# Kernel tuning notes

Hardware: AMD Instinct MI355X
Metric: run time of the kernel (lower is better)

Reference implementation:

```python
import jax, jax.numpy as jnp
import numpy as np

B, TE, TD, E, H, V, A, MAXOOV = 8, 400, 100, 128, 256, 50000, 612, 50
VEXT = V + MAXOOV


def setup_inputs():
    key = jax.random.key(0)
    it = iter(jax.random.split(key, 40))
    def nrm(shape, s=0.05):
        return jax.random.normal(next(it), shape, jnp.float32) * s
    inp = {
        "encoder_tokens": jax.random.randint(next(it), (B, TE), 0, V, dtype=jnp.int32),
        "decoder_tokens": jax.random.randint(next(it), (B, TD), 0, V, dtype=jnp.int32),
        "encoder_ext_tokens": jax.random.randint(next(it), (B, TE), 0, VEXT, dtype=jnp.int32),
        "encoder_mask": jnp.ones((B, TE), jnp.float32),
        "embedding": nrm((V, E)),
        "Wih_f": nrm((E, 4 * H)), "Whh_f": nrm((H, 4 * H)), "b_f": jnp.zeros((4 * H,), jnp.float32),
        "Wih_b": nrm((E, 4 * H)), "Whh_b": nrm((H, 4 * H)), "b_b": jnp.zeros((4 * H,), jnp.float32),
        "Wred": nrm((2 * H, H)), "bred": jnp.zeros((H,), jnp.float32),
        "Wenc_feat": nrm((2 * H, A)), "benc_feat": jnp.zeros((A,), jnp.float32),
        "v": nrm((A,), 1.0),
        "Wx": nrm((E + 2 * H, E)), "bx": jnp.zeros((E,), jnp.float32),
        "Wih_d": nrm((E, 4 * H)), "Whh_d": nrm((H, 4 * H)), "b_d": jnp.zeros((4 * H,), jnp.float32),
        "Wdf": nrm((TD, 2 * H, A)), "bdf": jnp.zeros((TD, A), jnp.float32),
        "Wpg": nrm((2 * H + H + H + E, 1)), "bpg": jnp.zeros((1,), jnp.float32),
        "Wout": nrm((H + 2 * H, H)), "bout": jnp.zeros((H,), jnp.float32),
        "Wv": nrm((H, V)), "bv": jnp.zeros((V,), jnp.float32),
    }
    return inp


def _lstm(xs, Wih, Whh, b):
    # xs: [T, B, E] -> outputs [T, B, H], final (h, c)
    def step(carry, x):
        h, c = carry
        g = x @ Wih + h @ Whh + b
        i, f, gg, o = jnp.split(g, 4, axis=-1)  # torch gate order i,f,g,o
        c = jax.nn.sigmoid(f) * c + jax.nn.sigmoid(i) * jnp.tanh(gg)
        h = jax.nn.sigmoid(o) * jnp.tanh(c)
        return (h, c), h
    z = jnp.zeros((xs.shape[1], Whh.shape[0]), xs.dtype)
    (hT, cT), hs = jax.lax.scan(step, (z, z), xs)
    return hs, hT, cT


def reference(encoder_tokens, decoder_tokens, encoder_ext_tokens, encoder_mask,
              embedding, Wih_f, Whh_f, b_f, Wih_b, Whh_b, b_b, Wred, bred,
              Wenc_feat, benc_feat, v, Wx, bx, Wih_d, Whh_d, b_d, Wdf, bdf,
              Wpg, bpg, Wout, bout, Wv, bv):
    # ---- bidirectional LSTM encoder (full-length sequences, mask == 1) ----
    enc_emb = embedding[encoder_tokens]               # [B, TE, E]
    xs = enc_emb.transpose(1, 0, 2)                   # [TE, B, E]
    hf, hTf, cTf = _lstm(xs, Wih_f, Whh_f, b_f)
    hb_rev, hTb, cTb = _lstm(xs[::-1], Wih_b, Whh_b, b_b)
    hb = hb_rev[::-1]
    enc_out = jnp.concatenate([hf, hb], -1).transpose(1, 0, 2)  # [B, TE, 2H]

    # ---- state reducer (original uses reduce_h_layer for BOTH h and c) ----
    h0 = jax.nn.relu(jnp.concatenate([hTf, hTb], -1) @ Wred + bred)
    c0 = jax.nn.relu(jnp.concatenate([cTf, cTb], -1) @ Wred + bred)

    # ---- 1x1 conv == linear on encoder states ----
    enc_feat = enc_out @ Wenc_feat + benc_feat        # [B, TE, A]

    dec_emb = embedding[decoder_tokens].transpose(1, 0, 2)  # [TD, B, E]

    def dec_step(carry, xs_t):
        h, c, ctx = carry
        emb_t, Wdf_t, bdf_t = xs_t
        x = jnp.concatenate([emb_t, ctx], -1) @ Wx + bx          # [B, E]
        g = x @ Wih_d + h @ Whh_d + b_d
        i, f, gg, o = jnp.split(g, 4, axis=-1)
        c = jax.nn.sigmoid(f) * c + jax.nn.sigmoid(i) * jnp.tanh(gg)
        h = jax.nn.sigmoid(o) * jnp.tanh(c)
        dec_feat = jnp.concatenate([h, c], -1) @ Wdf_t + bdf_t   # [B, A] (per-step weights)
        e = jnp.einsum('a,bta->bt', v, jnp.tanh(enc_feat + dec_feat[:, None, :]))
        attn = jax.nn.softmax(e, axis=-1) * encoder_mask
        attn = attn / attn.sum(-1, keepdims=True)
        ctx = jnp.einsum('bt,btd->bd', attn, enc_out)            # [B, 2H]
        p_gen = jax.nn.sigmoid(jnp.concatenate([ctx, h, c, x], -1) @ Wpg + bpg)  # [B, 1]
        out = jnp.concatenate([h, ctx], -1) @ Wout + bout        # [B, H]
        return (h, c, ctx), (out, attn, p_gen)

    ctx0 = jnp.zeros((enc_out.shape[0], 2 * H), enc_out.dtype)
    _, (outs, attns, pgens) = jax.lax.scan(dec_step, (h0, c0, ctx0), (dec_emb, Wdf, bdf))
    # outs [TD,B,H], attns [TD,B,TE], pgens [TD,B,1]

    # ---- pointer-generator mixture over extended vocab ----
    vocab_dist = jax.nn.softmax(outs @ Wv + bv, axis=-1)         # [TD, B, V]
    vocab_dist = pgens * vocab_dist
    attn_w = (1.0 - pgens) * attns                               # [TD, B, TE]

    def scatter_one(a, idx):
        return jnp.zeros((VEXT,), a.dtype).at[idx].add(a)
    copy_dist = jax.vmap(jax.vmap(scatter_one, in_axes=(0, 0)), in_axes=(0, None))(
        attn_w, encoder_ext_tokens)                              # [TD, B, VEXT]

    extra = jnp.zeros(vocab_dist.shape[:2] + (MAXOOV,), vocab_dist.dtype)
    final = jnp.concatenate([vocab_dist, extra], -1) + copy_dist # [TD, B, VEXT]
    return final
```

## Files before the change

### kernel.cpp

```cpp
#include <hip/hip_runtime.h>

#define DEVI __device__ __forceinline__

constexpr int B_ = 8, TE_ = 400, TD_ = 100, E_ = 128, H_ = 256;
constexpr int A_ = 612, V_ = 50000, VEXT_ = 50050;
constexpr int H4_ = 1024, H2_ = 512;
constexpr int NS_ = 16, SLW_ = 40;

constexpr size_t OFS_HBF  = 0;
constexpr size_t OFS_HBB  = 4096;
constexpr size_t OFS_CT   = 8192;
constexpr size_t OFS_CHC  = 12288;
constexpr size_t OFS_PG   = 32896;
constexpr size_t OFS_SROW = 33696;
constexpr size_t OFS_FLG  = 34496;
constexpr size_t OFS_ATT  = 35520;
constexpr size_t OFS_EO   = 355520;
constexpr size_t OFS_OUTS = OFS_EO;
constexpr size_t OFS_EF   = OFS_EO + (size_t)B_*TE_*H2_;

constexpr size_t DO_GINF = 0;
constexpr size_t DO_GINB = DO_GINF + (size_t)TE_*B_*H4_;
constexpr size_t DO_GDEC = DO_GINB + (size_t)TE_*B_*H4_;
constexpr size_t DO_XPRE = DO_GDEC + (size_t)TD_*B_*H4_;
constexpr size_t DO_CTXH = DO_XPRE + (size_t)TD_*B_*E_;
constexpr size_t DO_HCH  = DO_CTXH + (size_t)TD_*B_*H2_;
constexpr size_t DO_WCG  = DO_HCH + (size_t)TD_*B_*H2_;
constexpr size_t DO_EOWT = DO_WCG + (size_t)H2_*H4_;
constexpr size_t DO_EPB  = DO_EOWT + (size_t)B_*H4_*TE_;

#if defined(__has_builtin)
#if __has_builtin(__builtin_amdgcn_rcpf)
#define HAS_RCPF 1
#endif
#endif

DEVI float rcp_fast(float x) {
#ifdef HAS_RCPF
  return __builtin_amdgcn_rcpf(x);
#else
  return 1.0f / x;
#endif
}

DEVI float sigm(float x) { return rcp_fast(1.0f + __expf(-x)); }
DEVI float tanh_fast(float x) {
  float e = __expf(2.0f * x);
  return 1.0f - 2.0f * rcp_fast(e + 1.0f);
}

DEVI float ld_at(const float* p) {
  unsigned u = __hip_atomic_load((const unsigned*)p, __ATOMIC_RELAXED, __HIP_MEMORY_SCOPE_AGENT);
  return __uint_as_float(u);
}
DEVI void st_at(float* p, float v) {
  __hip_atomic_store((unsigned*)p, __float_as_uint(v), __ATOMIC_RELAXED, __HIP_MEMORY_SCOPE_AGENT);
}

#define WAIT_VM() do { asm volatile("s_waitcnt vmcnt(0)" ::: "memory"); \
                       __builtin_amdgcn_sched_barrier(0); } while (0)

DEVI float wave_max(float v) {
#pragma unroll
  for (int o = 32; o; o >>= 1) v = fmaxf(v, __shfl_xor(v, o));
  return v;
}
DEVI float wave_sum(float v) {
#pragma unroll
  for (int o = 32; o; o >>= 1) v += __shfl_xor(v, o);
  return v;
}

DEVI void flag_bar(unsigned* flags, int ncheck, int slot, unsigned ep, int stride) {
  __syncthreads();
  if (threadIdx.x == 0) {
    asm volatile("s_waitcnt vmcnt(0)" ::: "memory");
    __hip_atomic_store(&flags[slot * stride], ep, __ATOMIC_RELAXED, __HIP_MEMORY_SCOPE_AGENT);
  }
  if ((int)threadIdx.x < ncheck) {
    while (__hip_atomic_load(&flags[threadIdx.x * stride], __ATOMIC_RELAXED,
                             __HIP_MEMORY_SCOPE_AGENT) < ep) {
      __builtin_amdgcn_s_sleep(2);
    }
  }
  __syncthreads();
  asm volatile("" ::: "memory");
}

__global__ __launch_bounds__(256) void k0_wcg(
    const float* __restrict__ Wx, const float* __restrict__ Wih_d, float* __restrict__ dob)
{
  __shared__ float AsT[32 * 64];
  __shared__ float Bsh[32 * 64];
  const float* Am = Wx + 128 * 128;
  float* C = dob + DO_WCG;
  const int ct = blockIdx.x, rt = blockIdx.y, tid = threadIdx.x;
  const int c0 = ct * 64, r0 = rt * 64;
  const int tx = tid & 15, ty = tid >> 4;
  float4 acc0 = make_float4(0,0,0,0), acc1 = acc0, acc2 = acc0, acc3 = acc0;
  for (int kc = 0; kc < 4; ++kc) {
#pragma unroll
    for (int i = 0; i < 2; ++i) {
      int q = tid * 2 + i;
      int r = q >> 3, kq = q & 7;
      float4 v = *(const float4*)&Am[(size_t)(r0 + r) * 128 + kc * 32 + kq * 4];
      AsT[(kq * 4 + 0) * 64 + r] = v.x; AsT[(kq * 4 + 1) * 64 + r] = v.y;
      AsT[(kq * 4 + 2) * 64 + r] = v.z; AsT[(kq * 4 + 3) * 64 + r] = v.w;
    }
#pragma unroll
    for (int i = 0; i < 2; ++i) {
      int q = tid * 2 + i;
      int kk = q >> 4, cq = q & 15;
      *(float4*)&Bsh[kk * 64 + cq * 4] =
          *(const float4*)&Wih_d[(size_t)(kc * 32 + kk) * H4_ + c0 + cq * 4];
    }
    __syncthreads();
#pragma unroll
    for (int kk = 0; kk < 32; ++kk) {
      float4 w4 = *(float4*)&Bsh[kk * 64 + tx * 4];
      const float* ar = &AsT[kk * 64 + ty * 4];
      acc0.x += ar[0]*w4.x; acc0.y += ar[0]*w4.y; acc0.z += ar[0]*w4.z; acc0.w += ar[0]*w4.w;
      acc1.x += ar[1]*w4.x; acc1.y += ar[1]*w4.y; acc1.z += ar[1]*w4.z; acc1.w += ar[1]*w4.w;
      acc2.x += ar[2]*w4.x; acc2.y += ar[2]*w4.y; acc2.z += ar[2]*w4.z; acc2.w += ar[2]*w4.w;
      acc3.x += ar[3]*w4.x; acc3.y += ar[3]*w4.y; acc3.z += ar[3]*w4.z; acc3.w += ar[3]*w4.w;
    }
    __syncthreads();
  }
  float4 r4[4] = {acc0, acc1, acc2, acc3};
#pragma unroll
  for (int i = 0; i < 4; ++i)
    *(float4*)&C[(size_t)(r0 + ty * 4 + i) * H4_ + c0 + tx * 4] = r4[i];
}

__global__ __launch_bounds__(256) void k1_embed_gates(
    const int* __restrict__ etok, const float* __restrict__ emb,
    const float* __restrict__ Wih_f, const float* __restrict__ b_f,
    const float* __restrict__ Wih_b, const float* __restrict__ b_b,
    float* __restrict__ gin_f, float* __restrict__ gin_b, float* __restrict__ ws)
{
  __shared__ float er[8 * 128];
  const int t = blockIdx.x, tid = threadIdx.x;
  if (t == 0) {
    for (int i = tid; i < 8192; i += 256) ws[OFS_HBF + i] = 0.0f;
    unsigned* f = (unsigned*)(ws + OFS_FLG);
    for (int i = tid; i < 1024; i += 256) f[i] = 0u;
  }
  for (int i = tid; i < 1024; i += 256) {
    int b = i >> 7, e = i & 127;
    er[i] = emb[(size_t)etok[b * TE_ + t] * E_ + e];
  }
  __syncthreads();
  float bfv[4], bbv[4];
#pragma unroll
  for (int g = 0; g < 4; ++g) { bfv[g] = b_f[g * H_ + tid]; bbv[g] = b_b[g * H_ + tid]; }
  float af[32], ab[32];
#pragma unroll
  for (int i = 0; i < 32; ++i) { af[i] = bfv[i & 3]; ab[i] = bbv[i & 3]; }
  for (int e = 0; e < E_; ++e) {
    float wf[4], wb[4];
#pragma unroll
    for (int g = 0; g < 4; ++g) {
      wf[g] = Wih_f[(size_t)e * H4_ + g * H_ + tid];
      wb[g] = Wih_b[(size_t)e * H4_ + g * H_ + tid];
    }
#pragma unroll
    for (int b = 0; b < 8; ++b) {
      float x = er[b * 128 + e];
#pragma unroll
      for (int g = 0; g < 4; ++g) { af[b * 4 + g] += x * wf[g]; ab[b * 4 + g] += x * wb[g]; }
    }
  }
#pragma unroll
  for (int b = 0; b < 8; ++b)
#pragma unroll
    for (int g = 0; g < 4; ++g) {
      gin_f[((size_t)t * 8 + b) * H4_ + g * H_ + tid] = af[b * 4 + g];
      gin_b[((size_t)t * 8 + b) * H4_ + g * H_ + tid] = ab[b * 4 + g];
    }
}

__global__ __launch_bounds__(256) void k1d_dec_pre(
    const int* __restrict__ dtok, const float* __restrict__ emb,
    const float* __restrict__ Wx, const float* __restrict__ bx,
    const float* __restrict__ Wih_d, const float* __restrict__ b_d,
    float* __restrict__ dob)
{
  __shared__ float er[8 * 128];
  __shared__ float xl[8 * 128];
  const int t = blockIdx.x, tid = threadIdx.x;
  for (int i = tid; i < 1024; i += 256) {
    int b = i >> 7, e = i & 127;
    er[i] = emb[(size_t)dtok[b * TD_ + t] * E_ + e];
  }
  __syncthreads();
  {
    const int col = tid & 127, bh = tid >> 7;
#pragma unroll
    for (int ii = 0; ii < 4; ++ii) {
      int b = bh + (ii << 1);
      float acc = bx[col];
      for (int k = 0; k < 128; ++k) acc += er[b * 128 + k] * Wx[(size_t)k * E_ + col];
      xl[b * 128 + col] = acc;
      dob[DO_XPRE + ((size_t)t * 8 + b) * E_ + col] = acc;
    }
  }
  __syncthreads();
  float bv[4];
#pragma unroll
  for (int g = 0; g < 4; ++g) bv[g] = b_d[g * H_ + tid];
  float af[32];
#pragma unroll
  for (int i = 0; i < 32; ++i) af[i] = bv[i & 3];
  for (int e = 0; e < E_; ++e) {
    float w[4];
#pragma unroll
    for (int g = 0; g < 4; ++g) w[g] = Wih_d[(size_t)e * H4_ + g * H_ + tid];
#pragma unroll
    for (int b = 0; b < 8; ++b) {
      float x = xl[b * 128 + e];
#pragma unroll
      for (int g = 0; g < 4; ++g) af[b * 4 + g] += x * w[g];
    }
  }
#pragma unroll
  for (int b = 0; b < 8; ++b)
#pragma unroll
    for (int g = 0; g < 4; ++g)
      dob[DO_GDEC + ((size_t)t * 8 + b) * H4_ + g * H_ + tid] = af[b * 4 + g];
}

__global__ __launch_bounds__(256, 1) void k2_encoder_scan(
    const float* __restrict__ gin_f, const float* __restrict__ gin_b,
    const float* __restrict__ Whh_f, const float* __restrict__ Whh_b,
    float* __restrict__ ws)
{
  __shared__ float sm[4096];
  const int bid = blockIdx.x, tid = threadIdx.x;
  const int dir = bid >> 5, c0 = (bid & 31) * 8;
  const float* Whh = dir ? Whh_b : Whh_f;
  const float* gin = dir ? gin_b : gin_f;
  float* hb = ws + (dir ? OFS_HBB : OFS_HBF);
  float* cT = ws + OFS_CT;
  float* eo = ws + OFS_EO;
  unsigned* flg = (unsigned*)(ws + OFS_FLG) + (dir ? 128 : 0);
  const int slot = bid & 31;

  const int jl = tid >> 3, kg = tid & 7;
  const int gt = jl >> 3, hcl = jl & 7;
  const int jcol = gt * H_ + c0 + hcl;
  float wreg[32];
#pragma unroll
  for (int kk = 0; kk < 32; ++kk) wreg[kk] = Whh[(size_t)(kg + kk * 8) * H4_ + jcol];

  const int uhc = tid >> 3, ub = tid & 7;
  float c_reg = 0.0f;
  unsigned ep = 0;

  for (int t = 0; t < TE_; ++t) {
    const int te = dir ? (TE_ - 1 - t) : t;
    float* hrd = hb + (t & 1) * 2048;
    float* hwr = hb + ((t & 1) ^ 1) * 2048;
    float gpre[4] = {0, 0, 0, 0};
    if (tid < 64) {
#pragma unroll
      for (int gg = 0; gg < 4; ++gg)
        gpre[gg] = gin[((size_t)te * 8 + ub) * H4_ + gg * H_ + c0 + uhc];
    }
    {
      float4 v0, v1;
      const float* a0 = &hrd[tid * 8];
      const float* a1 = &hrd[tid * 8 + 4];
      asm volatile(
          "global_load_dwordx4 %0, %2, off sc0 sc1\n\t"
          "global_load_dwordx4 %1, %3, off sc0 sc1"
          : "=&v"(v0), "=&v"(v1) : "v"(a0), "v"(a1));
      WAIT_VM();
      *(float4*)&sm[tid * 8] = v0;
      *(float4*)&sm[tid * 8 + 4] = v1;
    }
    __syncthreads();
    float acc[8] = {0, 0, 0, 0, 0, 0, 0, 0};
#pragma unroll
    for (int kk = 0; kk < 32; ++kk) {
      float w = wreg[kk];
      const float* hp = &sm[(kg + kk * 8) * 8];
#pragma unroll
      for (int b = 0; b < 8; ++b) acc[b] += hp[b] * w;
    }
    float* part = sm + 2048;
    *(float4*)&part[(jl * 8 + kg) * 8]     = make_float4(acc[0], acc[1], acc[2], acc[3]);
    *(float4*)&part[(jl * 8 + kg) * 8 + 4] = make_float4(acc[4], acc[5], acc[6], acc[7]);
    __syncthreads();
    if (tid < 64) {
      float g[4];
#pragma unroll
      for (int gg = 0; gg < 4; ++gg) {
        float s = gpre[gg];
#pragma unroll
        for (int k2 = 0; k2 < 8; ++k2) s += part[((gg * 8 + uhc) * 8 + k2) * 8 + ub];
        g[gg] = s;
      }
      float ci = sigm(g[0]), cf = sigm(g[1]), cg = tanh_fast(g[2]), co = sigm(g[3]);
      c_reg = cf * c_reg + ci * cg;
      float hn = co * tanh_fast(c_reg);
      st_at(&hwr[(c0 + uhc) * 8 + ub], hn);
      eo[((size_t)ub * TE_ + te) * H2_ + dir * H_ + c0 + uhc] = hn;
      if (t == TE_ - 1) cT[ub * H2_ + dir * H_ + c0 + uhc] = c_reg;
    }
    ep++; flag_bar(flg, 32, slot, ep, 4);
  }
}

__global__ __launch_bounds__(256) void k3_encfeat(
    const float* __restrict__ eo, const float* __restrict__ Wef,
    const float* __restrict__ bef, float* __restrict__ ef)
{
  __shared__ float AsT[32 * 64];
  __shared__ float Wsh[32 * 64];
  const int ct = blockIdx.x, rt = blockIdx.y, tid = threadIdx.x;
  const int c0 = ct * 64, r0 = rt * 64;
  const int tx = tid & 15, ty = tid >> 4;
  float4 acc0 = make_float4(0,0,0,0), acc1 = acc0, acc2 = acc0, acc3 = acc0;
  for (int kc = 0; kc < 16; ++kc) {
#pragma unroll
    for (int i = 0; i < 2; ++i) {
      int q = tid * 2 + i;
      int r = q >> 3, kq = q & 7;
      float4 v = *(const float4*)&eo[(size_t)(r0 + r) * H2_ + kc * 32 + kq * 4];
      AsT[(kq * 4 + 0) * 64 + r] = v.x; AsT[(kq * 4 + 1) * 64 + r] = v.y;
      AsT[(kq * 4 + 2) * 64 + r] = v.z; AsT[(kq * 4 + 3) * 64 + r] = v.w;
    }
#pragma unroll
    for (int i = 0; i < 2; ++i) {
      int q = tid * 2 + i;
      int kk = q >> 4, cq = q & 15;
      int col = c0 + cq * 4;
      float4 v = make_float4(0,0,0,0);
      if (col < A_) v = *(const float4*)&Wef[(size_t)(kc * 32 + kk) * A_ + col];
      *(float4*)&Wsh[kk * 64 + cq * 4] = v;
    }
    __syncthreads();
#pragma unroll
    for (int kk = 0; kk < 32; ++kk) {
      float4 w4 = *(float4*)&Wsh[kk * 64 + tx * 4];
      const float* ar = &AsT[kk * 64 + ty * 4];
      acc0.x += ar[0]*w4.x; acc0.y += ar[0]*w4.y; acc0.z += ar[0]*w4.z; acc0.w += ar[0]*w4.w;
      acc1.x += ar[1]*w4.x; acc1.y += ar[1]*w4.y; acc1.z += ar[1]*w4.z; acc1.w += ar[1]*w4.w;
      acc2.x += ar[2]*w4.x; acc2.y += ar[2]*w4.y; acc2.z += ar[2]*w4.z; acc2.w += ar[2]*w4.w;
      acc3.x += ar[3]*w4.x; acc3.y += ar[3]*w4.y; acc3.z += ar[3]*w4.z; acc3.w += ar[3]*w4.w;
    }
    __syncthreads();
  }
  const int col = c0 + tx * 4;
  if (col < A_) {
    float4 bb = *(const float4*)&bef[col];
    float4 r4[4] = {acc0, acc1, acc2, acc3};
#pragma unroll
    for (int i = 0; i < 4; ++i) {
      int row = r0 + ty * 4 + i;
      float4 o = make_float4(r4[i].x + bb.x, r4[i].y + bb.y, r4[i].z + bb.z, r4[i].w + bb.w);
      *(float4*)&ef[(size_t)row * A_ + col] = o;
    }
  }
}

__global__ __launch_bounds__(256) void k3b_eowt(
    const float* __restrict__ eo, const float* __restrict__ dob_c, float* __restrict__ dob)
{
  __shared__ float Wt[32 * 64];
  __shared__ float Et[32 * 40];
  const float* Wcg = dob_c + DO_WCG;
  float* eoWT = dob + DO_EOWT;
  const int jt = blockIdx.x, tt = blockIdx.y, b = blockIdx.z, tid = threadIdx.x;
  const int j0 = jt * 64, te0 = tt * 40;
  const int j_l = tid & 63, tq = tid >> 6;
  float acc[10];
#pragma unroll
  for (int u = 0; u < 10; ++u) acc[u] = 0.0f;
  for (int kc = 0; kc < 16; ++kc) {
#pragma unroll
    for (int i = 0; i < 2; ++i) {
      int q = tid * 2 + i;
      int kk = q >> 4, j4 = q & 15;
      *(float4*)&Wt[kk * 64 + j4 * 4] =
          *(const float4*)&Wcg[(size_t)(kc * 32 + kk) * H4_ + j0 + j4 * 4];
    }
#pragma unroll
    for (int i = 0; i < 2; ++i) {
      int q = tid + i * 256;
      if (q < 320) {
        int te_l = q >> 3, kq = q & 7;
        float4 v = *(const float4*)&eo[((size_t)b * TE_ + te0 + te_l) * H2_ + kc * 32 + kq * 4];
        Et[(kq * 4 + 0) * 40 + te_l] = v.x; Et[(kq * 4 + 1) * 40 + te_l] = v.y;
        Et[(kq * 4 + 2) * 40 + te_l] = v.z; Et[(kq * 4 + 3) * 40 + te_l] = v.w;
      }
    }
    __syncthreads();
#pragma unroll
    for (int kk = 0; kk < 32; ++kk) {
      float w = Wt[kk * 64 + j_l];
      const float* ep2 = &Et[kk * 40 + tq * 10];
#pragma unroll
      for (int u = 0; u < 10; ++u) acc[u] += w * ep2[u];
    }
    __syncthreads();
  }
  float* outp = &eoWT[((size_t)b * H4_ + j0 + j_l) * TE_ + te0 + tq * 10];
#pragma unroll
  for (int u = 0; u < 10; ++u) outp[u] = acc[u];
}

__global__ __launch_bounds__(512, 1) void k4_decoder(
    const float* __restrict__ maskp,
    const float* __restrict__ Wred, const float* __restrict__ bred,
    const float* __restrict__ Whh_d,
    const float* __restrict__ Wdf, const float* __restrict__ bdf,
    const float* __restrict__ vvec, float* __restrict__ ws, float* __restrict__ dob)
{
  __shared__ float eoW[TE_ * 64];
  __shared__ float eu[TE_];
  __shared__ float hcL[512];
  __shared__ float red[16];
  __shared__ float gdL[64];
  __shared__ float gl[64];
  __shared__ float pgl[64 * 9];
  __shared__ float prt[1280];
  __shared__ float dfl[48];
  __shared__ float bdfL[48];
  __shared__ float vvL[48];

  float* chc = ws + OFS_CHC;
  float* att = ws + OFS_ATT;
  const float* efG = ws + OFS_EF;
  const float* hbf = ws + OFS_HBF;
  const float* hbb = ws + OFS_HBB;
  const float* cT  = ws + OFS_CT;
  unsigned* flgF = (unsigned*)(ws + OFS_FLG) + 256;
  const float* gdec = dob + DO_GDEC;
  const float* eoWT = dob + DO_EOWT;
  float* epb = dob + DO_EPB;
  float* hch = dob + DO_HCH;
  const int bid = blockIdx.x, tid = threadIdx.x;
  const int b = bid >> 4, s = bid & 15;
  unsigned* flgG = (unsigned*)(ws + OFS_FLG) + 512 + b * 64;
  const int a0 = s * SLW_, w = (s == 15) ? 12 : SLW_;
  const int nq = w >> 2;

  for (int i = tid; i < 64 * 100; i += 512) {
    int jgi = i / 100, c = i - jgi * 100;
    int jreal = (jgi >> 4) * 256 + s * 16 + (jgi & 15);
    float4 v = *(const float4*)&eoWT[((size_t)b * H4_ + jreal) * TE_ + c * 4];
    eoW[(c * 4 + 0) * 64 + jgi] = v.x;
    eoW[(c * 4 + 1) * 64 + jgi] = v.y;
    eoW[(c * 4 + 2) * 64 + jgi] = v.z;
    eoW[(c * 4 + 3) * 64 + jgi] = v.w;
  }
  const int jg = tid & 63, l8 = tid >> 6;
  const int jreal = (jg >> 4) * 256 + s * 16 + (jg & 15);
  float wreg[32];
#pragma unroll
  for (int kk = 0; kk < 32; ++kk)
    wreg[kk] = Whh_d[(size_t)(l8 + kk * 8) * H4_ + jreal];
  if (tid < w) vvL[tid] = vvec[a0 + tid];

  if (bid < 32) {
    const int isC = bid >> 4, pb = (bid >> 1) & 7, half = bid & 1;
    if (tid < 512)
      hcL[tid] = isC ? cT[pb * H2_ + tid]
                     : (tid < H_ ? hbf[tid * 8 + pb] : hbb[(tid - H_) * 8 + pb]);
    __syncthreads();
    {
      const int col_l = tid & 127, ks = tid >> 7;
      float acc = 0.0f;
      for (int kk = 0; kk < 128; ++kk) {
        int k = ks * 128 + kk;
        acc += hcL[k] * Wred[(size_t)k * H_ + half * 128 + col_l];
      }
      prt[ks * 128 + col_l] = acc;
    }
    __syncthreads();
    if (tid < 128) {
      float v2 = fmaxf(prt[tid] + prt[128 + tid] + prt[256 + tid] + prt[384 + tid] +
                       bred[half * 128 + tid], 0.0f);
      st_at(&chc[pb * H2_ + isC * H_ + half * 128 + tid], v2);
    }
  } else {
    float dm = 0.0f;
#pragma unroll
    for (int i = 0; i < 7; ++i) {
      int f = (bid - 32) * 3264 + i * 512 + tid;
      if (i * 512 + tid < 3264 && f < H2_ * A_) dm += Wdf[f];
    }
    asm volatile("" :: "v"(dm));
  }
  unsigned ep = 1;
  flag_bar(flgF, 128, bid, ep, 2);

  float c_reg = 0.0f;
  if (tid < 16) c_reg = ld_at(&chc[b * H2_ + H_ + s * 16 + tid]);
  unsigned epg = 0;

  for (int t = 0; t <= TD_; ++t) {
    const int cur = t & 1, nxt = cur ^ 1;

    {
      const int teA = (tid < TE_) ? tid : TE_ - 1;
      const int tcl = (t < TD_) ? t : TD_ - 1;
      const float* ae = &epb[((size_t)b * TE_ + teA) * 16];
      const float* ah = &chc[cur * 4096 + b * H2_ + (tid & 63) * 4];
      const int gi = tid & 15;
      const float* agd = &gdec[((size_t)tcl * 8 + b) * H4_ +
                               (gi >> 2) * 256 + s * 16 + (gi & 3) * 4];
      float4 v0, v1, v2, v3, vh, vgd;
      asm volatile(
          "global_load_dwordx4 %0, %6, off sc0 sc1\n\t"
          "global_load_dwordx4 %1, %7, off sc0 sc1\n\t"
          "global_load_dwordx4 %2, %8, off sc0 sc1\n\t"
          "global_load_dwordx4 %3, %9, off sc0 sc1\n\t"
          "global_load_dwordx4 %4, %10, off sc0 sc1\n\t"
          "global_load_dwordx4 %5, %11, off sc0 sc1"
          : "=&v"(v0), "=&v"(v1), "=&v"(v2), "=&v"(v3), "=&v"(vh), "=&v"(vgd)
          : "v"(ae), "v"(ae + 4), "v"(ae + 8), "v"(ae + 12), "v"(ah), "v"(agd));
      WAIT_VM();
      if (t > 0 && tid < TE_)
        eu[tid] = (v0.x + v0.y + v0.z + v0.w) + (v1.x + v1.y + v1.z + v1.w) +
                  (v2.x + v2.y + v2.z + v2.w) + (v3.x + v3.y + v3.z + v3.w);
      if (tid < 64) *(float4*)&hcL[tid * 4] = vh;
      if (tid < 16) *(float4*)&gdL[(gi >> 2) * 16 + (gi & 3) * 4] = vgd;
      __syncthreads();

      float inv = 0.0f;
      if (t > 0) {
        float m = (tid < TE_) ? eu[tid] : -3.4e38f;
        m = wave_max(m);
        if ((tid & 63) == 0) red[tid >> 6] = m;
        __syncthreads();
        m = red[0];
#pragma unroll
        for (int i = 1; i < 8; ++i) m = fmaxf(m, red[i]);
        float u = 0.0f;
        if (tid < TE_) {
          u = __expf(eu[tid] - m) * maskp[b * TE_ + tid];
          eu[tid] = u;
        }
        float sl = wave_sum(u);
        if ((tid & 63) == 0) red[8 + (tid >> 6)] = sl;
        __syncthreads();
        float S = 0.0f;
#pragma unroll
        for (int i = 0; i < 8; ++i) S += red[8 + i];
        inv = rcp_fast(S);
      }

      if (t > 0 && s == 0 && tid < TE_)
        att[((size_t)(t - 1) * 8 + b) * TE_ + tid] = eu[tid] * inv;

      if (t < TD_) {
        float accG = 0.0f, accW = 0.0f;
        if (t > 0) {
          for (int te = l8; te < TE_; te += 8)
            accG += eoW[te * 64 + jg] * eu[te];
        }
#pragma unroll
        for (int kk = 0; kk < 32; ++kk)
          accW += wreg[kk] * hcL[l8 + kk * 8];
        pgl[jg * 9 + l8] = accG * inv + accW;
        __syncthreads();
        if (tid < 64) {
          float sg = gdL[tid];
#pragma unroll
          for (int l = 0; l < 8; ++l) sg += pgl[tid * 9 + l];
          gl[tid] = sg;
        }
        __syncthreads();
        if (tid < 16) {
          float g0 = gl[tid], g1 = gl[16 + tid], g2 = gl[32 + tid], g3 = gl[48 + tid];
          float ci = sigm(g0), cf = sigm(g1), cg = tanh_fast(g2), co = sigm(g3);
          c_reg = cf * c_reg + ci * cg;
          float hn = co * tanh_fast(c_reg);
          int hc = s * 16 + tid;
          st_at(&chc[nxt * 4096 + b * H2_ + hc], hn);
          st_at(&chc[nxt * 4096 + b * H2_ + H_ + hc], c_reg);
          hch[((size_t)t * 8 + b) * H2_ + hc] = hn;
          hch[((size_t)t * 8 + b) * H2_ + H_ + hc] = c_reg;
        }
      }
    }
    if (t == TD_) break;
    epg++; flag_bar(flgG, 16, s, epg, 4);

    {
      {
        const float* ahc = &chc[nxt * 4096 + b * H2_ + (tid & 127) * 4];
        const int cl = (tid < 10) ? tid : 9;
        const float* abf = &bdf[(size_t)t * A_ + a0 + cl * 4];
        float4 vhc, vbf;
        asm volatile(
            "global_load_dwordx4 %0, %2, off sc0 sc1\n\t"
            "global_load_dwordx4 %1, %3, off sc0 sc1"
            : "=&v"(vhc), "=&v"(vbf) : "v"(ahc), "v"(abf));
        WAIT_VM();
        if (tid < 128) *(float4*)&hcL[tid * 4] = vhc;
        if (tid < 10) *(float4*)&bdfL[tid * 4] = vbf;
      }
      __syncthreads();

      const float* wp = Wdf + (size_t)t * H2_ * A_;
      {
        const int kq = tid >> 4, al = tid & 15;
        if (al < nq) {
          float4 a4 = make_float4(0, 0, 0, 0);
          const float* wpc = wp + a0 + al * 4;
#pragma unroll
          for (int i = 0; i < 16; ++i) {
            int k = kq * 16 + i;
            float4 w4 = *(const float4*)&wpc[(size_t)k * A_];
            float hv = hcL[k];
            a4.x += hv * w4.x; a4.y += hv * w4.y; a4.z += hv * w4.z; a4.w += hv * w4.w;
          }
          *(float4*)&prt[(kq * 10 + al) * 4] = a4;
        }
      }
      float dm = 0.0f;
      if (t + 1 < TD_) {
        const float* wp1 = Wdf + (size_t)(t + 1) * H2_ * A_ + (size_t)tid * A_ + a0;
#pragma unroll
        for (int q = 0; q < 10; ++q) {
          float4 vx = *(const float4*)&wp1[q * 4];
          dm += vx.x + vx.y + vx.z + vx.w;
        }
      }
      __syncthreads();
      if (tid < w) {
        float ssum = bdfL[tid];
        const int c4 = tid >> 2, r = tid & 3;
#pragma unroll
        for (int kq = 0; kq < 32; ++kq) ssum += prt[(kq * 10 + c4) * 4 + r];
        dfl[tid] = ssum;
      }
      __syncthreads();

      if (tid < TE_) {
        const float* efp = &efG[((size_t)b * TE_ + tid) * A_ + a0];
        float acc = 0.0f;
        for (int q = 0; q < nq; ++q) {
          float4 e4 = *(const float4*)&efp[q * 4];
          const float* dd = &dfl[q * 4];
          const float* vv = &vvL[q * 4];
          acc += vv[0] * tanh_fast(e4.x + dd[0]);
          acc += vv[1] * tanh_fast(e4.y + dd[1]);
          acc += vv[2] * tanh_fast(e4.z + dd[2]);
          acc += vv[3] * tanh_fast(e4.w + dd[3]);
        }
        st_at(&epb[((size_t)b * TE_ + tid) * 16 + s], acc);
      }
      asm volatile("" :: "v"(dm));
    }
    epg++; flag_bar(flgG, 16, s, epg, 4);
  }
}

__global__ __launch_bounds__(256) void k4c_ctx(
    const float* __restrict__ ws, float* __restrict__ dob)
{
  __shared__ float AsT[32 * 64];
  __shared__ float Bsh[32 * 64];
  const float* att = ws + OFS_ATT;
  const float* eo  = ws + OFS_EO;
  float* ctxh = dob + DO_CTXH;
  const int ct = blockIdx.x, rt = blockIdx.y, b = blockIdx.z, tid = threadIdx.x;
  const int c0 = ct * 64, r0 = rt * 64;
  const int tx = tid & 15, ty = tid >> 4;
  float4 acc0 = make_float4(0,0,0,0), acc1 = acc0, acc2 = acc0, acc3 = acc0;
  for (int kc = 0; kc < 13; ++kc) {
#pragma unroll
    for (int i = 0; i < 2; ++i) {
      int q = tid * 2 + i;
      int r = q >> 3, kq = q & 7;
      int k = kc * 32 + kq * 4;
      float4 v = make_float4(0, 0, 0, 0);
      if (k < TE_ && r0 + r < TD_)
        v = *(const float4*)&att[((size_t)(r0 + r) * 8 + b) * TE_ + k];
      AsT[(kq * 4 + 0) * 64 + r] = v.x; AsT[(kq * 4 + 1) * 64 + r] = v.y;
      AsT[(kq * 4 + 2) * 64 + r] = v.z; AsT[(kq * 4 + 3) * 64 + r] = v.w;
    }
#pragma unroll
    for (int i = 0; i < 2; ++i) {
      int q = tid * 2 + i;
      int kk = q >> 4, cq = q & 15;
      int k = kc * 32 + kk;
      float4 v = make_float4(0, 0, 0, 0);
      if (k < TE_) v = *(const float4*)&eo[((size_t)b * TE_ + k) * H2_ + c0 + cq * 4];
      *(float4*)&Bsh[kk * 64 + cq * 4] = v;
    }
    __syncthreads();
#pragma unroll
    for (int kk = 0; kk < 32; ++kk) {
      float4 w4 = *(float4*)&Bsh[kk * 64 + tx * 4];
      const float* ar = &AsT[kk * 64 + ty * 4];
      acc0.x += ar[0]*w4.x; acc0.y += ar[0]*w4.y; acc0.z += ar[0]*w4.z; acc0.w += ar[0]*w4.w;
      acc1.x += ar[1]*w4.x; acc1.y += ar[1]*w4.y; acc1.z += ar[1]*w4.z; acc1.w += ar[1]*w4.w;
      acc2.x += ar[2]*w4.x; acc2.y += ar[2]*w4.y; acc2.z += ar[2]*w4.z; acc2.w += ar[2]*w4.w;
      acc3.x += ar[3]*w4.x; acc3.y += ar[3]*w4.y; acc3.z += ar[3]*w4.z; acc3.w += ar[3]*w4.w;
    }
    __syncthreads();
  }
  float4 r4[4] = {acc0, acc1, acc2, acc3};
#pragma unroll
  for (int i = 0; i < 4; ++i) {
    int row = r0 + ty * 4 + i;
    if (row < TD_)
      *(float4*)&ctxh[((size_t)row * 8 + b) * H2_ + c0 + tx * 4] = r4[i];
  }
}

__global__ __launch_bounds__(256) void k4b_post(
    const float* __restrict__ Wx, const float* __restrict__ Wout, const float* __restrict__ bout,
    const float* __restrict__ Wpg, const float* __restrict__ bpg,
    float* __restrict__ ws, const float* __restrict__ dob)
{
  __shared__ float hcl[4096], ctxl[4096], cpl[4096], xl[1024], red2[256];
  const int t = blockIdx.x, tid = threadIdx.x;
  const float* hch  = dob + DO_HCH;
  const float* ctxh = dob + DO_CTXH;
  const float* xpre = dob + DO_XPRE;
  for (int i = tid; i < 4096; i += 256) {
    hcl[i]  = hch[(size_t)t * 4096 + i];
    ctxl[i] = ctxh[(size_t)t * 4096 + i];
    cpl[i]  = t ? ctxh[(size_t)(t - 1) * 4096 + i] : 0.0f;
  }
  __syncthreads();
  {
    const int col = tid & 127, bh = tid >> 7;
#pragma unroll
    for (int ii = 0; ii < 4; ++ii) {
      int b = bh + (ii << 1);
      float acc = xpre[(size_t)t * 1024 + b * E_ + col];
      for (int k = 0; k < H2_; ++k) acc += cpl[b * H2_ + k] * Wx[(size_t)(128 + k) * E_ + col];
      xl[b * E_ + col] = acc;
    }
  }
  __syncthreads();
  {
    const int col = tid;
    for (int b = 0; b < 8; ++b) {
      float acc = bout[col];
      for (int k = 0; k < 768; ++k)
        acc += (k < H_ ? hcl[b * H2_ + k] : ctxl[b * H2_ + (k - H_)]) * Wout[(size_t)k * H_ + col];
      ws[OFS_OUTS + ((size_t)t * 8 + b) * H_ + col] = acc;
    }
  }
  {
    const int b = tid >> 5, sg = tid & 31;
    float acc = 0.0f;
    for (int j = 0; j < 36; ++j) {
      int k = sg * 36 + j;
      float xv;
      if (k < H2_)       xv = ctxl[b * H2_ + k];
      else if (k < 768)  xv = hcl[b * H2_ + (k - H2_)];
      else if (k < 1024) xv = hcl[b * H2_ + H_ + (k - 768)];
      else               xv = xl[b * E_ + (k - 1024)];
      acc += xv * Wpg[k];
    }
    red2[tid] = acc;
    __syncthreads();
    if (tid < 8) {
      float s = 0.0f;
      for (int k2 = 0; k2 < 32; ++k2) s += red2[tid * 32 + k2];
      ws[OFS_PG + t * 8 + tid] = sigm(s + bpg[0]);
    }
  }
}

__global__ __launch_bounds__(256) void k5a_logits(
    const float* __restrict__ outs, const float* __restrict__ Wv,
    const float* __restrict__ bv, float* __restrict__ out)
{
  __shared__ float aT[32 * 64];
  __shared__ float wl[32 * 256];
  const int ct = blockIdx.x, rt = blockIdx.y, tid = threadIdx.x;
  const int r0 = rt * 64, c0 = ct * 256;
  const int cq = tid & 63, rg = tid >> 6;
  float4 acc[16];
#pragma unroll
  for (int i = 0; i < 16; ++i) acc[i] = make_float4(0, 0, 0, 0);
  for (int kc = 0; kc < 8; ++kc) {
#pragma unroll
    for (int i = 0; i < 2; ++i) {
      int q = tid * 2 + i;
      int r = q >> 3, kq = q & 7;
      float4 v = make_float4(0, 0, 0, 0);
      if (r0 + r < 800) v = *(const float4*)&outs[(size_t)(r0 + r) * H_ + kc * 32 + kq * 4];
      aT[(kq * 4 + 0) * 64 + r] = v.x; aT[(kq * 4 + 1) * 64 + r] = v.y;
      aT[(kq * 4 + 2) * 64 + r] = v.z; aT[(kq * 4 + 3) * 64 + r] = v.w;
    }
#pragma unroll
    for (int i = 0; i < 8; ++i) {
      int q = tid + i * 256;
      int kk = q >> 6, c4 = q & 63;
      int col = c0 + c4 * 4;
      float4 v = make_float4(0, 0, 0, 0);
      if (col < V_) v = *(const float4*)&Wv[(size_t)(kc * 32 + kk) * V_ + col];
      *(float4*)&wl[kk * 256 + c4 * 4] = v;
    }
    __syncthreads();
#pragma unroll
    for (int kk = 0; kk < 32; ++kk) {
      float4 w4 = *(float4*)&wl[kk * 256 + cq * 4];
      const float* ar = &aT[kk * 64 + rg * 16];
#pragma unroll
      for (int rr = 0; rr < 16; ++rr) {
        float a = ar[rr];
        acc[rr].x += a * w4.x; acc[rr].y += a * w4.y;
        acc[rr].z += a * w4.z; acc[rr].w += a * w4.w;
      }
    }
    __syncthreads();
  }
  const int col = c0 + cq * 4;
  if (col < V_) {
    float4 bb = *(const float4*)&bv[col];
#pragma unroll
    for (int rr = 0; rr < 16; ++rr) {
      int row = r0 + rg * 16 + rr;
      if (row < 800) {
        float2 lo = make_float2(acc[rr].x + bb.x, acc[rr].y + bb.y);
        float2 hi = make_float2(acc[rr].z + bb.z, acc[rr].w + bb.w);
        *(float2*)&out[(size_t)row * VEXT_ + col] = lo;
        *(float2*)&out[(size_t)row * VEXT_ + col + 2] = hi;
      }
    }
  }
}

__global__ __launch_bounds__(256) void k5b_rowsum(const float* __restrict__ out, float* __restrict__ Srow)
{
  __shared__ float red[256];
  const int r = blockIdx.x, tid = threadIdx.x;
  const float* base = out + (size_t)r * VEXT_;
  float s = 0.0f;
  for (int i = tid; i < V_ / 2; i += 256) {
    float2 v = *(const float2*)&base[i * 2];
    s += __expf(v.x) + __expf(v.y);
  }
  red[tid] = s; __syncthreads();
  for (int st = 128; st > 0; st >>= 1) { if (tid < st) red[tid] += red[tid + st]; __syncthreads(); }
  if (tid == 0) Srow[r] = red[0];
}

__global__ __launch_bounds__(256) void k5c_final(
    float* __restrict__ out, const float* __restrict__ Srow, const float* __restrict__ pg)
{
  const int cc = blockIdx.x, r = blockIdx.y, tid = threadIdx.x;
  const float scale = pg[r] * rcp_fast(Srow[r]);
  float* base = out + (size_t)r * VEXT_;
#pragma unroll
  for (int i = 0; i < 4; ++i) {
    int col = cc * 2048 + i * 512 + tid * 2;
    if (col < V_) {
      float2 v = *(float2*)&base[col];
      v.x = __expf(v.x) * scale; v.y = __expf(v.y) * scale;
      *(float2*)&base[col] = v;
    } else if (col < VEXT_) {
      *(float2*)&base[col] = make_float2(0.0f, 0.0f);
    }
  }
}

__global__ __launch_bounds__(256) void k5d_scatter(
    float* __restrict__ out, const float* __restrict__ ws, const int* __restrict__ ext)
{
  const int r = blockIdx.x, tid = threadIdx.x;
  const int b = r & 7;
  const float* at = ws + OFS_ATT + (size_t)r * TE_;
  const float w = 1.0f - ws[OFS_PG + r];
  float* base = out + (size_t)r * VEXT_;
  for (int i = tid; i < TE_; i += 256)
    atomicAdd(&base[ext[b * TE_ + i]], w * at[i]);
}

extern "C" void kernel_launch(void* const* d_in, const int* in_sizes, int n_in,
                              void* d_out, int out_size, void* d_ws, size_t ws_size,
                              hipStream_t stream) {
  const int*   etok  = (const int*)d_in[0];
  const int*   dtok  = (const int*)d_in[1];
  const int*   ext   = (const int*)d_in[2];
  const float* maskp = (const float*)d_in[3];
  const float* emb   = (const float*)d_in[4];
  const float* Wih_f = (const float*)d_in[5];
  const float* Whh_f = (const float*)d_in[6];
  const float* b_f   = (const float*)d_in[7];
  const float* Wih_b = (const float*)d_in[8];
  const float* Whh_b = (const float*)d_in[9];
  const float* b_b   = (const float*)d_in[10];
  const float* Wred  = (const float*)d_in[11];
  const float* bred  = (const float*)d_in[12];
  const float* Wef   = (const float*)d_in[13];
  const float* bef   = (const float*)d_in[14];
  const float* vvec  = (const float*)d_in[15];
  const float* Wx    = (const float*)d_in[16];
  const float* bx    = (const float*)d_in[17];
  const float* Wih_d = (const float*)d_in[18];
  const float* Whh_d = (const float*)d_in[19];
  const float* b_d   = (const float*)d_in[20];
  const float* Wdf   = (const float*)d_in[21];
  const float* bdf   = (const float*)d_in[22];
  const float* Wpg   = (const float*)d_in[23];
  const float* bpg   = (const float*)d_in[24];
  const float* Wout  = (const float*)d_in[25];
  const float* bout  = (const float*)d_in[26];
  const float* Wv    = (const float*)d_in[27];
  const float* bv    = (const float*)d_in[28];
  float* out = (float*)d_out;
  float* wsf = (float*)d_ws;
  float* dob = out;

  float* gin_f = dob + DO_GINF;
  float* gin_b = dob + DO_GINB;

  k1_embed_gates<<<400, 256, 0, stream>>>(etok, emb, Wih_f, b_f, Wih_b, b_b, gin_f, gin_b, wsf);
  k0_wcg<<<dim3(16, 8), 256, 0, stream>>>(Wx, Wih_d, dob);
  k1d_dec_pre<<<100, 256, 0, stream>>>(dtok, emb, Wx, bx, Wih_d, b_d, dob);

  {
    void* args2[5] = {(void*)&gin_f, (void*)&gin_b, (void*)&Whh_f, (void*)&Whh_b, (void*)&wsf};
    if (hipLaunchCooperativeKernel((void*)k2_encoder_scan, dim3(64), dim3(256), args2, 0, stream) != hipSuccess)
      k2_encoder_scan<<<64, 256, 0, stream>>>(gin_f, gin_b, Whh_f, Whh_b, wsf);
  }

  k3_encfeat<<<dim3(10, 50), 256, 0, stream>>>(wsf + OFS_EO, Wef, bef, wsf + OFS_EF);
  k3b_eowt<<<dim3(16, 10, 8), 256, 0, stream>>>(wsf + OFS_EO, dob, dob);

  {
    void* args4[9] = {(void*)&maskp, (void*)&Wred, (void*)&bred, (void*)&Whh_d,
                      (void*)&Wdf, (void*)&bdf, (void*)&vvec, (void*)&wsf, (void*)&dob};
    if (hipLaunchCooperativeKernel((void*)k4_decoder, dim3(128), dim3(512), args4, 0, stream) != hipSuccess)
      k4_decoder<<<128, 512, 0, stream>>>(maskp, Wred, bred, Whh_d, Wdf, bdf, vvec, wsf, dob);
  }

  k4c_ctx<<<dim3(8, 2, 8), 256, 0, stream>>>(wsf, dob);
  k4b_post<<<100, 256, 0, stream>>>(Wx, Wout, bout, Wpg, bpg, wsf, dob);

  k5a_logits<<<dim3(196, 13), 256, 0, stream>>>(wsf + OFS_OUTS, Wv, bv, out);
  k5b_rowsum<<<800, 256, 0, stream>>>(out, wsf + OFS_SROW);
  k5c_final<<<dim3(25, 800), 256, 0, stream>>>(out, wsf + OFS_SROW, wsf + OFS_PG);
  k5d_scatter<<<800, 256, 0, stream>>>(out, wsf, ext);
}
```

Before: 3.766 ms.

## Fuse encoder input projection into scan, redistribute decoder loads, swap logits grid order

The separate embedding/input-gate kernel is removed. Its work moves into the cooperative encoder scan, which keeps Wih columns in registers and gathers embeddings per step. This drops the large gate-preactivation buffer write and read, but adds per-step input-projection work on the serial critical path. The decoder also spreads the attention store and the Wdf prefetch-touch across more threads, and the logits grid swaps its axes so row tiles vary fastest.

```diff
diff --git a/kernel.cpp b/kernel.cpp
--- a/kernel.cpp
+++ b/kernel.cpp
@@ -19,9 +19,7 @@
 constexpr size_t OFS_OUTS = OFS_EO;
 constexpr size_t OFS_EF   = OFS_EO + (size_t)B_*TE_*H2_;
 
-constexpr size_t DO_GINF = 0;
-constexpr size_t DO_GINB = DO_GINF + (size_t)TE_*B_*H4_;
-constexpr size_t DO_GDEC = DO_GINB + (size_t)TE_*B_*H4_;
+constexpr size_t DO_GDEC = 2ull*(size_t)TE_*B_*H4_;
 constexpr size_t DO_XPRE = DO_GDEC + (size_t)TD_*B_*H4_;
 constexpr size_t DO_CTXH = DO_XPRE + (size_t)TD_*B_*E_;
 constexpr size_t DO_HCH  = DO_CTXH + (size_t)TD_*B_*H2_;
@@ -88,13 +86,19 @@
 }
 
 __global__ __launch_bounds__(256) void k0_wcg(
-    const float* __restrict__ Wx, const float* __restrict__ Wih_d, float* __restrict__ dob)
+    const float* __restrict__ Wx, const float* __restrict__ Wih_d,
+    float* __restrict__ dob, float* __restrict__ ws)
 {
   __shared__ float AsT[32 * 64];
   __shared__ float Bsh[32 * 64];
   const float* Am = Wx + 128 * 128;
   float* C = dob + DO_WCG;
   const int ct = blockIdx.x, rt = blockIdx.y, tid = threadIdx.x;
+  if (ct == 0 && rt == 0) {
+    for (int i = tid; i < 8192; i += 256) ws[OFS_HBF + i] = 0.0f;
+    unsigned* f = (unsigned*)(ws + OFS_FLG);
+    for (int i = tid; i < 1024; i += 256) f[i] = 0u;
+  }
   const int c0 = ct * 64, r0 = rt * 64;
   const int tx = tid & 15, ty = tid >> 4;
   float4 acc0 = make_float4(0,0,0,0), acc1 = acc0, acc2 = acc0, acc3 = acc0;
@@ -132,53 +136,6 @@
     *(float4*)&C[(size_t)(r0 + ty * 4 + i) * H4_ + c0 + tx * 4] = r4[i];
 }
 
-__global__ __launch_bounds__(256) void k1_embed_gates(
-    const int* __restrict__ etok, const float* __restrict__ emb,
-    const float* __restrict__ Wih_f, const float* __restrict__ b_f,
-    const float* __restrict__ Wih_b, const float* __restrict__ b_b,
-    float* __restrict__ gin_f, float* __restrict__ gin_b, float* __restrict__ ws)
-{
-  __shared__ float er[8 * 128];
-  const int t = blockIdx.x, tid = threadIdx.x;
-  if (t == 0) {
-    for (int i = tid; i < 8192; i += 256) ws[OFS_HBF + i] = 0.0f;
-    unsigned* f = (unsigned*)(ws + OFS_FLG);
-    for (int i = tid; i < 1024; i += 256) f[i] = 0u;
-  }
-  for (int i = tid; i < 1024; i += 256) {
-    int b = i >> 7, e = i & 127;
-    er[i] = emb[(size_t)etok[b * TE_ + t] * E_ + e];
-  }
-  __syncthreads();
-  float bfv[4], bbv[4];
-#pragma unroll
-  for (int g = 0; g < 4; ++g) { bfv[g] = b_f[g * H_ + tid]; bbv[g] = b_b[g * H_ + tid]; }
-  float af[32], ab[32];
-#pragma unroll
-  for (int i = 0; i < 32; ++i) { af[i] = bfv[i & 3]; ab[i] = bbv[i & 3]; }
-  for (int e = 0; e < E_; ++e) {
-    float wf[4], wb[4];
-#pragma unroll
-    for (int g = 0; g < 4; ++g) {
-      wf[g] = Wih_f[(size_t)e * H4_ + g * H_ + tid];
-      wb[g] = Wih_b[(size_t)e * H4_ + g * H_ + tid];
-    }
-#pragma unroll
-    for (int b = 0; b < 8; ++b) {
-      float x = er[b * 128 + e];
-#pragma unroll
-      for (int g = 0; g < 4; ++g) { af[b * 4 + g] += x * wf[g]; ab[b * 4 + g] += x * wb[g]; }
-    }
-  }
-#pragma unroll
-  for (int b = 0; b < 8; ++b)
-#pragma unroll
-    for (int g = 0; g < 4; ++g) {
-      gin_f[((size_t)t * 8 + b) * H4_ + g * H_ + tid] = af[b * 4 + g];
-      gin_b[((size_t)t * 8 + b) * H4_ + g * H_ + tid] = ab[b * 4 + g];
-    }
-}
-
 __global__ __launch_bounds__(256) void k1d_dec_pre(
     const int* __restrict__ dtok, const float* __restrict__ emb,
     const float* __restrict__ Wx, const float* __restrict__ bx,
@@ -230,54 +187,64 @@
 }
 
 __global__ __launch_bounds__(256, 1) void k2_encoder_scan(
-    const float* __restrict__ gin_f, const float* __restrict__ gin_b,
+    const int* __restrict__ etok, const float* __restrict__ emb,
+    const float* __restrict__ Wih_f, const float* __restrict__ b_f,
+    const float* __restrict__ Wih_b, const float* __restrict__ b_b,
     const float* __restrict__ Whh_f, const float* __restrict__ Whh_b,
     float* __restrict__ ws)
 {
-  __shared__ float sm[4096];
+  __shared__ float sm[3072];
+  __shared__ float part[2048];
+  __shared__ int tokL[B_ * TE_];
   const int bid = blockIdx.x, tid = threadIdx.x;
   const int dir = bid >> 5, c0 = (bid & 31) * 8;
   const float* Whh = dir ? Whh_b : Whh_f;
-  const float* gin = dir ? gin_b : gin_f;
+  const float* Wih = dir ? Wih_b : Wih_f;
+  const float* bbp = dir ? b_b : b_f;
   float* hb = ws + (dir ? OFS_HBB : OFS_HBF);
   float* cT = ws + OFS_CT;
   float* eo = ws + OFS_EO;
   unsigned* flg = (unsigned*)(ws + OFS_FLG) + (dir ? 128 : 0);
   const int slot = bid & 31;
 
+  for (int i = tid; i < B_ * TE_; i += 256) tokL[i] = etok[i];
+
   const int jl = tid >> 3, kg = tid & 7;
   const int gt = jl >> 3, hcl = jl & 7;
   const int jcol = gt * H_ + c0 + hcl;
-  float wreg[32];
-#pragma unroll
-  for (int kk = 0; kk < 32; ++kk) wreg[kk] = Whh[(size_t)(kg + kk * 8) * H4_ + jcol];
-
+  float wreg[48];
+#pragma unroll
+  for (int kk = 0; kk < 48; ++kk) {
+    if (kk < 32) wreg[kk] = Whh[(size_t)(kg + kk * 8) * H4_ + jcol];
+    else         wreg[kk] = Wih[(size_t)(kg + (kk - 32) * 8) * H4_ + jcol];
+  }
   const int uhc = tid >> 3, ub = tid & 7;
+  float bias[4] = {0, 0, 0, 0};
+  if (tid < 64) {
+#pragma unroll
+    for (int g = 0; g < 4; ++g) bias[g] = bbp[g * H_ + c0 + uhc];
+  }
+  const int ebb = tid >> 5, e4 = tid & 31;
   float c_reg = 0.0f;
   unsigned ep = 0;
+  __syncthreads();
 
   for (int t = 0; t < TE_; ++t) {
     const int te = dir ? (TE_ - 1 - t) : t;
     float* hrd = hb + (t & 1) * 2048;
     float* hwr = hb + ((t & 1) ^ 1) * 2048;
-    float gpre[4] = {0, 0, 0, 0};
-    if (tid < 64) {
-#pragma unroll
-      for (int gg = 0; gg < 4; ++gg)
-        gpre[gg] = gin[((size_t)te * 8 + ub) * H4_ + gg * H_ + c0 + uhc];
-    }
-    {
-      float4 v0, v1;
-      const float* a0 = &hrd[tid * 8];
-      const float* a1 = &hrd[tid * 8 + 4];
-      asm volatile(
-          "global_load_dwordx4 %0, %2, off sc0 sc1\n\t"
-          "global_load_dwordx4 %1, %3, off sc0 sc1"
-          : "=&v"(v0), "=&v"(v1) : "v"(a0), "v"(a1));
-      WAIT_VM();
-      *(float4*)&sm[tid * 8] = v0;
-      *(float4*)&sm[tid * 8 + 4] = v1;
-    }
+    float4 ev = *(const float4*)&emb[(size_t)tokL[ebb * TE_ + te] * E_ + e4 * 4];
+    float4 v0, v1;
+    const float* a0p = &hrd[tid * 8];
+    const float* a1p = &hrd[tid * 8 + 4];
+    asm volatile(
+        "global_load_dwordx4 %0, %2, off sc0 sc1\n\t"
+        "global_load_dwordx4 %1, %3, off sc0 sc1"
+        : "=&v"(v0), "=&v"(v1) : "v"(a0p), "v"(a1p));
+    WAIT_VM();
+    *(float4*)&sm[tid * 8] = v0;
+    *(float4*)&sm[tid * 8 + 4] = v1;
+    *(float4*)&sm[2048 + ebb * 128 + e4 * 4] = ev;
     __syncthreads();
     float acc[8] = {0, 0, 0, 0, 0, 0, 0, 0};
 #pragma unroll
@@ -287,7 +254,13 @@
 #pragma unroll
       for (int b = 0; b < 8; ++b) acc[b] += hp[b] * w;
     }
-    float* part = sm + 2048;
+#pragma unroll
+    for (int kk = 32; kk < 48; ++kk) {
+      float w = wreg[kk];
+      const int e = kg + (kk - 32) * 8;
+#pragma unroll
+      for (int b = 0; b < 8; ++b) acc[b] += sm[2048 + b * 128 + e] * w;
+    }
     *(float4*)&part[(jl * 8 + kg) * 8]     = make_float4(acc[0], acc[1], acc[2], acc[3]);
     *(float4*)&part[(jl * 8 + kg) * 8 + 4] = make_float4(acc[4], acc[5], acc[6], acc[7]);
     __syncthreads();
@@ -295,7 +268,7 @@
       float g[4];
 #pragma unroll
       for (int gg = 0; gg < 4; ++gg) {
-        float s = gpre[gg];
+        float s = bias[gg];
 #pragma unroll
         for (int k2 = 0; k2 < 8; ++k2) s += part[((gg * 8 + uhc) * 8 + k2) * 8 + ub];
         g[gg] = s;
@@ -552,8 +525,8 @@
         inv = rcp_fast(S);
       }
 
-      if (t > 0 && s == 0 && tid < TE_)
-        att[((size_t)(t - 1) * 8 + b) * TE_ + tid] = eu[tid] * inv;
+      if (t > 0 && tid < 25)
+        att[((size_t)(t - 1) * 8 + b) * TE_ + s * 25 + tid] = eu[s * 25 + tid] * inv;
 
       if (t < TD_) {
         float accG = 0.0f, accW = 0.0f;
@@ -623,11 +596,17 @@
       }
       float dm = 0.0f;
       if (t + 1 < TD_) {
-        const float* wp1 = Wdf + (size_t)(t + 1) * H2_ * A_ + (size_t)tid * A_ + a0;
-#pragma unroll
-        for (int q = 0; q < 10; ++q) {
-          float4 vx = *(const float4*)&wp1[q * 4];
-          dm += vx.x + vx.y + vx.z + vx.w;
+        const float* wp1 = Wdf + (size_t)(t + 1) * H2_ * A_;
+#pragma unroll
+        for (int q = 0; q < 2; ++q) {
+          int f = tid + q * 512;
+          if (f < 640) {
+            int r = f / 10, c4 = f - r * 10;
+            if (c4 < nq) {
+              float4 vx = *(const float4*)&wp1[(size_t)(b * 64 + r) * A_ + a0 + c4 * 4];
+              dm += vx.x + vx.y + vx.z + vx.w;
+            }
+          }
         }
       }
       __syncthreads();
@@ -778,7 +757,7 @@
 {
   __shared__ float aT[32 * 64];
   __shared__ float wl[32 * 256];
-  const int ct = blockIdx.x, rt = blockIdx.y, tid = threadIdx.x;
+  const int rt = blockIdx.x, ct = blockIdx.y, tid = threadIdx.x;
   const int r0 = rt * 64, c0 = ct * 256;
   const int cq = tid & 63, rg = tid >> 6;
   float4 acc[16];
@@ -915,17 +894,14 @@
   float* wsf = (float*)d_ws;
   float* dob = out;
 
-  float* gin_f = dob + DO_GINF;
-  float* gin_b = dob + DO_GINB;
-
-  k1_embed_gates<<<400, 256, 0, stream>>>(etok, emb, Wih_f, b_f, Wih_b, b_b, gin_f, gin_b, wsf);
-  k0_wcg<<<dim3(16, 8), 256, 0, stream>>>(Wx, Wih_d, dob);
+  k0_wcg<<<dim3(16, 8), 256, 0, stream>>>(Wx, Wih_d, dob, wsf);
   k1d_dec_pre<<<100, 256, 0, stream>>>(dtok, emb, Wx, bx, Wih_d, b_d, dob);
 
   {
-    void* args2[5] = {(void*)&gin_f, (void*)&gin_b, (void*)&Whh_f, (void*)&Whh_b, (void*)&wsf};
+    void* args2[9] = {(void*)&etok, (void*)&emb, (void*)&Wih_f, (void*)&b_f,
+                      (void*)&Wih_b, (void*)&b_b, (void*)&Whh_f, (void*)&Whh_b, (void*)&wsf};
     if (hipLaunchCooperativeKernel((void*)k2_encoder_scan, dim3(64), dim3(256), args2, 0, stream) != hipSuccess)
-      k2_encoder_scan<<<64, 256, 0, stream>>>(gin_f, gin_b, Whh_f, Whh_b, wsf);
+      k2_encoder_scan<<<64, 256, 0, stream>>>(etok, emb, Wih_f, b_f, Wih_b, b_b, Whh_f, Whh_b, wsf);
   }
 
   k3_encfeat<<<dim3(10, 50), 256, 0, stream>>>(wsf + OFS_EO, Wef, bef, wsf + OFS_EF);
@@ -941,7 +917,7 @@
   k4c_ctx<<<dim3(8, 2, 8), 256, 0, stream>>>(wsf, dob);
   k4b_post<<<100, 256, 0, stream>>>(Wx, Wout, bout, Wpg, bpg, wsf, dob);
 
-  k5a_logits<<<dim3(196, 13), 256, 0, stream>>>(wsf + OFS_OUTS, Wv, bv, out);
+  k5a_logits<<<dim3(13, 196), 256, 0, stream>>>(wsf + OFS_OUTS, Wv, bv, out);
   k5b_rowsum<<<800, 256, 0, stream>>>(out, wsf + OFS_SROW);
   k5c_final<<<dim3(25, 800), 256, 0, stream>>>(out, wsf + OFS_SROW, wsf + OFS_PG);
   k5d_scatter<<<800, 256, 0, stream>>>(out, wsf, ext);
```

Result: no change. 3.734 ms (-0.8%).
